# Kernel tuning notes

Measured on AMD Instinct MI355X. Metric: run time of the kernel, lower is better.

## Reference

```python
import jax, jax.numpy as jnp
import numpy as np

N = 12288   # nodes
E = 393216  # edges (avg degree 32)
B = 16      # graphs in batch
F_IN = 15   # node feature dim
H = 32      # hidden_dim
EMB = 64    # embedding_dim
NC = 11     # num_classes
EDIM = 2    # edge feature dim
EPS = 1e-5  # BatchNorm eps


def _bn(x, gamma, beta):
    # training-mode BatchNorm1d: biased batch variance, matches torch normalization
    mu = jnp.mean(x, axis=0)
    var = jnp.var(x, axis=0)
    return gamma * (x - mu) * jax.lax.rsqrt(var + EPS) + beta


def setup_inputs() -> dict:
    key = jax.random.key(0)
    ks = jax.random.split(key, 16)
    def p(k, shape, s=0.05):
        return jax.random.normal(k, shape, dtype=jnp.float32) * s
    z = lambda *s: jnp.zeros(s, jnp.float32)
    o = lambda *s: jnp.ones(s, jnp.float32)
    return {
        "x": jax.random.normal(ks[0], (N, F_IN), dtype=jnp.float32),
        "edge_attr": jax.random.normal(ks[1], (E, EDIM), dtype=jnp.float32),
        "w_edge": p(ks[2], (EDIM, 1)), "b_edge": z(1),
        "w1": p(ks[3], (F_IN, H)), "b1": z(H), "g1": o(H), "be1": z(H),
        "w2": p(ks[4], (H, 2 * H)), "b2": z(2 * H), "g2": o(2 * H), "be2": z(2 * H),
        "w3": p(ks[5], (2 * H, EMB)), "b3": z(EMB), "g3": o(EMB), "be3": z(EMB),
        "wf1": p(ks[6], (EMB, 512)), "bf1": z(512), "gf1": o(512), "bef1": z(512),
        "wf2": p(ks[7], (512, 256)), "bf2": z(256), "gf2": o(256), "bef2": z(256),
        "wf3": p(ks[8], (256, NC)), "bf3": z(NC),
        "edge_index": jax.random.randint(ks[9], (2, E), 0, N, dtype=jnp.int64)
                      if jax.config.jax_enable_x64 else jax.random.randint(ks[9], (2, E), 0, N),
        "batch": jnp.sort(jax.random.randint(ks[10], (N,), 0, B)),
    }


def reference(x, edge_attr, w_edge, b_edge,
              w1, b1, g1, be1, w2, b2, g2, be2, w3, b3, g3, be3,
              wf1, bf1, gf1, bef1, wf2, bf2, gf2, bef2, wf3, bf3,
              edge_index, batch):
    # edge weights: sigmoid(Linear(edge_attr)) -> [E]
    ew = jax.nn.sigmoid(edge_attr @ w_edge + b_edge)[:, 0]
    # dense adjacency with self loops, accumulate duplicates (sparse_coo.to_dense)
    loop = jnp.arange(N)
    row = jnp.concatenate([edge_index[0], loop])
    col = jnp.concatenate([edge_index[1], loop])
    w_aug = jnp.concatenate([ew, jnp.ones((N,), ew.dtype)])
    adj = jnp.zeros((N, N), ew.dtype).at[row, col].add(w_aug)
    # symmetric degree normalization D^-1/2 A D^-1/2
    deg = adj.sum(axis=1)
    dis = jnp.where(deg > 0, jax.lax.rsqrt(jnp.where(deg > 0, deg, 1.0)), 0.0)
    support = dis[:, None] * adj * dis[None, :]
    # three GCN layers: support @ x @ W + b, BN, relu
    h = jax.nn.relu(_bn(support @ x @ w1 + b1, g1, be1))
    h = jax.nn.relu(_bn(support @ h @ w2 + b2, g2, be2))
    h = jax.nn.relu(_bn(support @ h @ w3 + b3, g3, be3))
    # global max pool per graph (empty graphs -> zeros)
    seg = jax.ops.segment_max(h, batch, num_segments=B)
    cnt = jax.ops.segment_sum(jnp.ones((N,), h.dtype), batch, num_segments=B)
    emb = jnp.where(cnt[:, None] > 0, seg, 0.0)
    # MLP head (dropout = identity at inference)
    o = jax.nn.relu(_bn(emb @ wf1 + bf1, gf1, bef1))
    o = jax.nn.relu(_bn(o @ wf2 + bf2, gf2, bef2))
    logits = o @ wf3 + bf3
    return jax.nn.log_softmax(logits, axis=1), emb
```

## Files before the change

kernel.cpp:

```cpp
#include <hip/hip_runtime.h>
#include <hip/hip_bf16.h>

#define NN   12288
#define EE   393216
#define WELL 96
#define NELL (NN*WELL)
#define BG   16
#define FIN  15
#define FH1  32
#define FH2  64
#define NCL  11
#define BNEPS 1e-5f
#define NBANK 32

typedef unsigned long long u64;
static inline int cdiv(long a, long b){ return (int)((a + b - 1) / b); }

__device__ __forceinline__ int getIdx(const void* p, long i, int is64){
  return is64 ? (int)((const long long*)p)[i] : ((const int*)p)[i];
}

__device__ __forceinline__ float degOf(u64 dc){
  return 1.0f + (float)(unsigned)(dc & 0xffffffffull) * (1.0f/1048576.0f);
}

__global__ void k_pre(u64* deg_cnt, uint4* csr_q, float* csp1, float* csp2,
                      float* csp3, const void* ei, const void* batch, int* flags){
  int g = blockIdx.x*256 + threadIdx.x;
  if (g < NELL/2) csr_q[g] = make_uint4(0,0,0,0);
  if (g < NN) deg_cnt[g] = 0ull;
  if (g < NBANK*128){ csp1[g] = 0.f; csp2[g] = 0.f; csp3[g] = 0.f; }
  if (blockIdx.x == 0 && threadIdx.x < 64){
    const int* a = (const int*)ei;
    unsigned long long m0 = __ballot(a[2*threadIdx.x + 1] == 0);
    const int* b = (const int*)batch;
    int j = 96*threadIdx.x;
    unsigned long long m1 = __ballot(b[2*j + 1] == 0);
    if (threadIdx.x == 0){
      flags[0] = (m0 == ~0ull) ? 1 : 0;
      flags[1] = (m1 == ~0ull) ? 1 : 0;
    }
  }
}

__global__ void k_edge(const float* ea, const float* we, const float* bedg,
                       const void* ei, const int* flags, u64* deg_cnt, u64* csr_p){
  int e = blockIdx.x*256 + threadIdx.x;
  if (e >= EE) return;
  int is64 = flags[0];
  float z = ea[2*e]*we[0] + ea[2*e+1]*we[1] + bedg[0];
  float w = 1.0f/(1.0f + expf(-z));
  int r = getIdx(ei, e, is64);
  int c = getIdx(ei, (long)EE + e, is64);
  u64 add = (1ull << 32) | (u64)__float2uint_rn(w * 1048576.0f);
  u64 old = atomicAdd(&deg_cnt[r], add);
  int slot = (int)(old >> 32);
  if (slot < WELL)
    csr_p[r*WELL + slot] = (u64)(unsigned)c | ((u64)__float_as_uint(w) << 32);
}

__global__ void k_fix(u64* csr_p, const u64* deg_cnt){
  int g = blockIdx.x*256 + threadIdx.x;
  if (g >= NELL) return;
  u64 v = csr_p[g];
  unsigned wu = (unsigned)(v >> 32);
  if (wu == 0u) return;
  int c = (int)(unsigned)(v & 0xffffffffull);
  float w = __uint_as_float(wu) * rsqrtf(degOf(deg_cnt[c]));
  ((unsigned*)csr_p)[2*g + 1] = __float_as_uint(w);
}

template<int F, int FP, int FO, int APPLY_BN>
__global__ void __launch_bounds__(256) k_layer(
    const float* __restrict__ Hin, const float* __restrict__ csin,
    const float* __restrict__ g, const float* __restrict__ be,
    const float* __restrict__ W, const float* __restrict__ bias,
    const u64* __restrict__ deg_cnt, const u64* __restrict__ csr_p,
    float* __restrict__ Pout, float* __restrict__ csout){
  const int R = 256/FP;
  __shared__ float At[R][FP];
  __shared__ float lcs[FO], lcq[FO];
  if (threadIdx.x < FO){ lcs[threadIdx.x] = 0.f; lcq[threadIdx.x] = 0.f; }
  int f = threadIdx.x % FP, lr = threadIdx.x / FP;
  float sc = 1.f, sh = 0.f;
  if (APPLY_BN && f < F){
    float s = 0.f, q = 0.f;
    #pragma unroll
    for (int b = 0; b < NBANK; b++){ s += csin[b*128 + f]; q += csin[b*128 + 64 + f]; }
    float mu  = s*(1.0f/NN);
    float var = q*(1.0f/NN) - mu*mu;
    float rinv = rsqrtf(var + BNEPS);
    sc = g[f]*rinv; sh = be[f] - mu*sc;
  }
  int row = blockIdx.x*R + lr;
  if (f < F){
    u64 dc = deg_cnt[row];
    float d = rsqrtf(degOf(dc));
    int n = (int)(dc >> 32);
    float v0 = Hin[row*F + f];
    if (APPLY_BN) v0 = fmaxf(v0*sc + sh, 0.f);
    float acc = d * v0;
    int nch = (n + 7) >> 3;
    const uint4* pb = (const uint4*)(csr_p + row*WELL);
    if (nch > 0){
      uint4 a0 = pb[0], a1 = pb[1], a2 = pb[2], a3 = pb[3];
      for (int ch = 0; ch < nch; ch++){
        uint4 b0, b1, b2, b3;
        bool more = (ch + 1 < nch);
        if (more){ b0 = pb[4*ch+4]; b1 = pb[4*ch+5]; b2 = pb[4*ch+6]; b3 = pb[4*ch+7]; }
        float h0 = Hin[(int)a0.x*F + f];
        float h1 = Hin[(int)a0.z*F + f];
        float h2 = Hin[(int)a1.x*F + f];
        float h3 = Hin[(int)a1.z*F + f];
        float h4 = Hin[(int)a2.x*F + f];
        float h5 = Hin[(int)a2.z*F + f];
        float h6 = Hin[(int)a3.x*F + f];
        float h7 = Hin[(int)a3.z*F + f];
        if (APPLY_BN){
          h0 = fmaxf(h0*sc + sh, 0.f); h1 = fmaxf(h1*sc + sh, 0.f);
          h2 = fmaxf(h2*sc + sh, 0.f); h3 = fmaxf(h3*sc + sh, 0.f);
          h4 = fmaxf(h4*sc + sh, 0.f); h5 = fmaxf(h5*sc + sh, 0.f);
          h6 = fmaxf(h6*sc + sh, 0.f); h7 = fmaxf(h7*sc + sh, 0.f);
        }
        acc += __uint_as_float(a0.y)*h0 + __uint_as_float(a0.w)*h1
             + __uint_as_float(a1.y)*h2 + __uint_as_float(a1.w)*h3
             + __uint_as_float(a2.y)*h4 + __uint_as_float(a2.w)*h5
             + __uint_as_float(a3.y)*h6 + __uint_as_float(a3.w)*h7;
        if (more){ a0 = b0; a1 = b1; a2 = b2; a3 = b3; }
      }
    }
    At[lr][f] = d * acc;
  }
  __syncthreads();
  const int fo = threadIdx.x % FO;
  float bb = bias[fo];
  for (int o = threadIdx.x; o < R*FO; o += 256){
    int l = o / FO;
    float s = bb;
    #pragma unroll
    for (int fi = 0; fi < F; fi++) s += At[l][fi] * W[fi*FO + fo];
    Pout[(blockIdx.x*R + l)*FO + fo] = s;
    atomicAdd(&lcs[fo], s);
    atomicAdd(&lcq[fo], s*s);
  }
  __syncthreads();
  if (threadIdx.x < FO){
    int bank = blockIdx.x & (NBANK-1);
    atomicAdd(&csout[bank*128 + threadIdx.x],      lcs[threadIdx.x]);
    atomicAdd(&csout[bank*128 + 64 + threadIdx.x], lcq[threadIdx.x]);
  }
}

__global__ void k_pool(const float* P3, const float* cs3, const float* g3,
                       const float* be3, const void* batch, const int* flags,
                       float* embf, float* out){
  int is64 = flags[1];
  int b = blockIdx.x;
  int lo = 0, hi = NN;
  while (lo < hi){ int m = (lo+hi)>>1; if (getIdx(batch, m, is64) < b) lo = m+1; else hi = m; }
  int start = lo;
  lo = start; hi = NN;
  while (lo < hi){ int m = (lo+hi)>>1; if (getIdx(batch, m, is64) < b+1) lo = m+1; else hi = m; }
  int end = lo;
  int f = threadIdx.x & 63, grp = threadIdx.x >> 6;
  float s = 0.f, q = 0.f;
  #pragma unroll
  for (int bk = 0; bk < NBANK; bk++){ s += cs3[bk*128 + f]; q += cs3[bk*128 + 64 + f]; }
  float mu  = s*(1.0f/NN);
  float var = q*(1.0f/NN) - mu*mu;
  float rinv = rsqrtf(var + BNEPS);
  float sc = g3[f]*rinv, sh = be3[f] - mu*sc;
  float m = 0.0f;
  for (int i = start + grp; i < end; i += 4)
    m = fmaxf(m, P3[(long)i*FH2 + f]*sc + sh);
  __shared__ float shm[4][64];
  shm[grp][f] = m;
  __syncthreads();
  if (grp == 0){
    float v = fmaxf(fmaxf(shm[0][f], shm[1][f]), fmaxf(shm[2][f], shm[3][f]));
    embf[b*64 + f] = v;
    out[BG*NCL + b*64 + f] = v;
  }
}

__global__ void __launch_bounds__(256) k_fcA(const float* embf, const float* wf1,
    const float* bf1, const float* gf1, const float* bef1, float* s1g){
  int c = blockIdx.x*4 + (threadIdx.x >> 6);
  int l = threadIdx.x & 63;
  float wcol = wf1[l*512 + c];
  float z[BG];
  #pragma unroll
  for (int r = 0; r < BG; r++){
    float v = embf[r*64 + l] * wcol;
    #pragma unroll
    for (int off = 32; off > 0; off >>= 1) v += __shfl_down(v, off);
    z[r] = v;
  }
  if (l == 0){
    float bb = bf1[c];
    float s = 0.f, q = 0.f;
    #pragma unroll
    for (int r = 0; r < BG; r++){ float zr = z[r] + bb; s += zr; q += zr*zr; }
    float mean = s*(1.f/BG), var = q*(1.f/BG) - mean*mean;
    float inv = rsqrtf(var + BNEPS);
    float gg = gf1[c], b2 = bef1[c];
    #pragma unroll
    for (int r = 0; r < BG; r++)
      s1g[r*512 + c] = fmaxf(gg*(z[r] + bb - mean)*inv + b2, 0.f);
  }
}

__global__ void __launch_bounds__(256) k_fcB(const float* s1g, const float* wf2,
    const float* bf2, const float* gf2, const float* bef2, float* s2g){
  int c = blockIdx.x*4 + (threadIdx.x >> 6);
  int l = threadIdx.x & 63;
  float wreg[8];
  #pragma unroll
  for (int j = 0; j < 8; j++) wreg[j] = wf2[(l + 64*j)*256 + c];
  float z[BG];
  #pragma unroll
  for (int r = 0; r < BG; r++){
    float v = 0.f;
    #pragma unroll
    for (int j = 0; j < 8; j++) v += s1g[r*512 + l + 64*j] * wreg[j];
    #pragma unroll
    for (int off = 32; off > 0; off >>= 1) v += __shfl_down(v, off);
    z[r] = v;
  }
  if (l == 0){
    float bb = bf2[c];
    float s = 0.f, q = 0.f;
    #pragma unroll
    for (int r = 0; r < BG; r++){ float zr = z[r] + bb; s += zr; q += zr*zr; }
    float mean = s*(1.f/BG), var = q*(1.f/BG) - mean*mean;
    float inv = rsqrtf(var + BNEPS);
    float gg = gf2[c], b2 = bef2[c];
    #pragma unroll
    for (int r = 0; r < BG; r++)
      s2g[r*256 + c] = fmaxf(gg*(z[r] + bb - mean)*inv + b2, 0.f);
  }
}

__global__ void k_fc3(const float* s2g, const float* wf3, const float* bf3, float* out){
  __shared__ float s2[BG*256];
  __shared__ float sl[BG*NCL];
  int t = threadIdx.x;
  for (int i = t; i < BG*256; i += 256) s2[i] = s2g[i];
  __syncthreads();
  if (t < BG*NCL){
    int r = t / NCL, c = t - r*NCL;
    float s = bf3[c];
    for (int k = 0; k < 256; k++) s += s2[r*256 + k]*wf3[k*NCL + c];
    sl[t] = s;
  }
  __syncthreads();
  if (t < BG){
    float m = -1e30f;
    for (int c = 0; c < NCL; c++) m = fmaxf(m, sl[t*NCL + c]);
    float s = 0.f;
    for (int c = 0; c < NCL; c++) s += expf(sl[t*NCL + c] - m);
    float lg = logf(s) + m;
    for (int c = 0; c < NCL; c++) out[t*NCL + c] = sl[t*NCL + c] - lg;
  }
}

extern "C" void kernel_launch(void* const* d_in, const int* in_sizes, int n_in,
                              void* d_out, int out_size, void* d_ws, size_t ws_size,
                              hipStream_t stream){
  const float* x    = (const float*)d_in[0];
  const float* ea   = (const float*)d_in[1];
  const float* we   = (const float*)d_in[2];
  const float* bedg = (const float*)d_in[3];
  const float* w1   = (const float*)d_in[4];  const float* b1  = (const float*)d_in[5];
  const float* g1   = (const float*)d_in[6];  const float* be1 = (const float*)d_in[7];
  const float* w2   = (const float*)d_in[8];  const float* b2  = (const float*)d_in[9];
  const float* g2   = (const float*)d_in[10]; const float* be2 = (const float*)d_in[11];
  const float* w3   = (const float*)d_in[12]; const float* b3  = (const float*)d_in[13];
  const float* g3   = (const float*)d_in[14]; const float* be3 = (const float*)d_in[15];
  const float* wf1  = (const float*)d_in[16]; const float* bf1 = (const float*)d_in[17];
  const float* gf1  = (const float*)d_in[18]; const float* bef1= (const float*)d_in[19];
  const float* wf2  = (const float*)d_in[20]; const float* bf2 = (const float*)d_in[21];
  const float* gf2  = (const float*)d_in[22]; const float* bef2= (const float*)d_in[23];
  const float* wf3  = (const float*)d_in[24]; const float* bf3 = (const float*)d_in[25];
  const void* ei    = d_in[26];
  const void* batch = d_in[27];
  float* out = (float*)d_out;

  u64* wq = (u64*)d_ws;
  u64* deg_cnt = wq; wq += NN;
  u64* csr_p   = wq; wq += NELL;
  float* ws = (float*)wq;
  float* P1    = ws; ws += NN*FH1;
  float* P2    = ws; ws += NN*FH2;
  float* P3    = ws; ws += NN*FH2;
  float* csp1  = ws; ws += NBANK*128;
  float* csp2  = ws; ws += NBANK*128;
  float* csp3  = ws; ws += NBANK*128;
  float* embf  = ws; ws += BG*64;
  float* s1g   = ws; ws += BG*512;
  float* s2g   = ws; ws += BG*256;
  int* flags   = (int*)ws;

  k_pre<<<cdiv(NELL/2,256), 256, 0, stream>>>(deg_cnt, (uint4*)csr_p,
                                              csp1, csp2, csp3, ei, batch, flags);
  k_edge<<<cdiv(EE,256), 256, 0, stream>>>(ea, we, bedg, ei, flags, deg_cnt, csr_p);
  k_fix<<<cdiv(NELL,256), 256, 0, stream>>>(csr_p, deg_cnt);

  k_layer<FIN,16,FH1,0><<<NN/16, 256, 0, stream>>>(x, nullptr, nullptr, nullptr,
      w1, b1, deg_cnt, csr_p, P1, csp1);
  k_layer<FH1,32,FH2,1><<<NN/8, 256, 0, stream>>>(P1, csp1, g1, be1,
      w2, b2, deg_cnt, csr_p, P2, csp2);
  k_layer<FH2,64,FH2,1><<<NN/4, 256, 0, stream>>>(P2, csp2, g2, be2,
      w3, b3, deg_cnt, csr_p, P3, csp3);

  k_pool<<<BG, 256, 0, stream>>>(P3, csp3, g3, be3, batch, flags, embf, out);
  k_fcA<<<128, 256, 0, stream>>>(embf, wf1, bf1, gf1, bef1, s1g);
  k_fcB<<<64, 256, 0, stream>>>(s1g, wf2, bf2, gf2, bef2, s2g);
  k_fc3<<<1, 256, 0, stream>>>(s2g, wf3, bf3, out);
}
```

Measured before the change: 265.7 us.

## Drop ELL zero-fill, bound slots by degree count, fuse MLP tail cooperatively

The full zeroing pass over the padded ELL adjacency buffer is removed. k_fix and the layer gathers now bound each row by its atomic edge count and mask stale slots, instead of relying on zero-filled entries. The ELL width grows to 128 so row offsets can be computed with shifts. The pool and three MLP kernels are merged into one 16-block cooperative kernel that uses grid syncs, cutting launch overhead, and the edge-attribute read is vectorized. The cost is a larger workspace and extra per-chunk masking branches in the layer kernels.

```diff
diff --git a/kernel.cpp b/kernel.cpp
--- a/kernel.cpp
+++ b/kernel.cpp
@@ -1,9 +1,12 @@
 #include <hip/hip_runtime.h>
+#include <hip/hip_cooperative_groups.h>
 #include <hip/hip_bf16.h>
+
+namespace cg = cooperative_groups;
 
 #define NN   12288
 #define EE   393216
-#define WELL 96
+#define WELL 128
 #define NELL (NN*WELL)
 #define BG   16
 #define FIN  15
@@ -24,10 +27,9 @@
   return 1.0f + (float)(unsigned)(dc & 0xffffffffull) * (1.0f/1048576.0f);
 }
 
-__global__ void k_pre(u64* deg_cnt, uint4* csr_q, float* csp1, float* csp2,
-                      float* csp3, const void* ei, const void* batch, int* flags){
+__global__ void k_pre(u64* deg_cnt, float* csp1, float* csp2, float* csp3,
+                      const void* ei, const void* batch, int* flags){
   int g = blockIdx.x*256 + threadIdx.x;
-  if (g < NELL/2) csr_q[g] = make_uint4(0,0,0,0);
   if (g < NN) deg_cnt[g] = 0ull;
   if (g < NBANK*128){ csp1[g] = 0.f; csp2[g] = 0.f; csp3[g] = 0.f; }
   if (blockIdx.x == 0 && threadIdx.x < 64){
@@ -48,7 +50,8 @@
   int e = blockIdx.x*256 + threadIdx.x;
   if (e >= EE) return;
   int is64 = flags[0];
-  float z = ea[2*e]*we[0] + ea[2*e+1]*we[1] + bedg[0];
+  float2 eav = ((const float2*)ea)[e];
+  float z = eav.x*we[0] + eav.y*we[1] + bedg[0];
   float w = 1.0f/(1.0f + expf(-z));
   int r = getIdx(ei, e, is64);
   int c = getIdx(ei, (long)EE + e, is64);
@@ -56,17 +59,19 @@
   u64 old = atomicAdd(&deg_cnt[r], add);
   int slot = (int)(old >> 32);
   if (slot < WELL)
-    csr_p[r*WELL + slot] = (u64)(unsigned)c | ((u64)__float_as_uint(w) << 32);
+    csr_p[(r << 7) + slot] = (u64)(unsigned)c | ((u64)__float_as_uint(w) << 32);
 }
 
 __global__ void k_fix(u64* csr_p, const u64* deg_cnt){
   int g = blockIdx.x*256 + threadIdx.x;
   if (g >= NELL) return;
+  int row = g >> 7, s = g & (WELL-1);
+  int n = (int)(deg_cnt[row] >> 32);
+  n = n < WELL ? n : WELL;
+  if (s >= n) return;
   u64 v = csr_p[g];
-  unsigned wu = (unsigned)(v >> 32);
-  if (wu == 0u) return;
   int c = (int)(unsigned)(v & 0xffffffffull);
-  float w = __uint_as_float(wu) * rsqrtf(degOf(deg_cnt[c]));
+  float w = __uint_as_float((unsigned)(v >> 32)) * rsqrtf(degOf(deg_cnt[c]));
   ((unsigned*)csr_p)[2*g + 1] = __float_as_uint(w);
 }
 
@@ -97,17 +102,29 @@
     u64 dc = deg_cnt[row];
     float d = rsqrtf(degOf(dc));
     int n = (int)(dc >> 32);
+    n = n < WELL ? n : WELL;
     float v0 = Hin[row*F + f];
     if (APPLY_BN) v0 = fmaxf(v0*sc + sh, 0.f);
     float acc = d * v0;
     int nch = (n + 7) >> 3;
-    const uint4* pb = (const uint4*)(csr_p + row*WELL);
+    const uint4* pb = (const uint4*)(csr_p + ((long)row << 7));
     if (nch > 0){
       uint4 a0 = pb[0], a1 = pb[1], a2 = pb[2], a3 = pb[3];
       for (int ch = 0; ch < nch; ch++){
         uint4 b0, b1, b2, b3;
         bool more = (ch + 1 < nch);
         if (more){ b0 = pb[4*ch+4]; b1 = pb[4*ch+5]; b2 = pb[4*ch+6]; b3 = pb[4*ch+7]; }
+        int base = ch*8;
+        if (base + 8 > n){
+          if (base+0 >= n){ a0.x = 0u; a0.y = 0u; }
+          if (base+1 >= n){ a0.z = 0u; a0.w = 0u; }
+          if (base+2 >= n){ a1.x = 0u; a1.y = 0u; }
+          if (base+3 >= n){ a1.z = 0u; a1.w = 0u; }
+          if (base+4 >= n){ a2.x = 0u; a2.y = 0u; }
+          if (base+5 >= n){ a2.z = 0u; a2.w = 0u; }
+          if (base+6 >= n){ a3.x = 0u; a3.y = 0u; }
+          if (base+7 >= n){ a3.z = 0u; a3.w = 0u; }
+        }
         float h0 = Hin[(int)a0.x*F + f];
         float h1 = Hin[(int)a0.z*F + f];
         float h2 = Hin[(int)a1.x*F + f];
@@ -151,116 +168,138 @@
   }
 }
 
-__global__ void k_pool(const float* P3, const float* cs3, const float* g3,
-                       const float* be3, const void* batch, const int* flags,
-                       float* embf, float* out){
-  int is64 = flags[1];
-  int b = blockIdx.x;
-  int lo = 0, hi = NN;
-  while (lo < hi){ int m = (lo+hi)>>1; if (getIdx(batch, m, is64) < b) lo = m+1; else hi = m; }
-  int start = lo;
-  lo = start; hi = NN;
-  while (lo < hi){ int m = (lo+hi)>>1; if (getIdx(batch, m, is64) < b+1) lo = m+1; else hi = m; }
-  int end = lo;
-  int f = threadIdx.x & 63, grp = threadIdx.x >> 6;
-  float s = 0.f, q = 0.f;
-  #pragma unroll
-  for (int bk = 0; bk < NBANK; bk++){ s += cs3[bk*128 + f]; q += cs3[bk*128 + 64 + f]; }
-  float mu  = s*(1.0f/NN);
-  float var = q*(1.0f/NN) - mu*mu;
-  float rinv = rsqrtf(var + BNEPS);
-  float sc = g3[f]*rinv, sh = be3[f] - mu*sc;
-  float m = 0.0f;
-  for (int i = start + grp; i < end; i += 4)
-    m = fmaxf(m, P3[(long)i*FH2 + f]*sc + sh);
-  __shared__ float shm[4][64];
-  shm[grp][f] = m;
-  __syncthreads();
-  if (grp == 0){
-    float v = fmaxf(fmaxf(shm[0][f], shm[1][f]), fmaxf(shm[2][f], shm[3][f]));
-    embf[b*64 + f] = v;
-    out[BG*NCL + b*64 + f] = v;
-  }
-}
-
-__global__ void __launch_bounds__(256) k_fcA(const float* embf, const float* wf1,
-    const float* bf1, const float* gf1, const float* bef1, float* s1g){
-  int c = blockIdx.x*4 + (threadIdx.x >> 6);
-  int l = threadIdx.x & 63;
-  float wcol = wf1[l*512 + c];
-  float z[BG];
-  #pragma unroll
-  for (int r = 0; r < BG; r++){
-    float v = embf[r*64 + l] * wcol;
-    #pragma unroll
-    for (int off = 32; off > 0; off >>= 1) v += __shfl_down(v, off);
-    z[r] = v;
-  }
-  if (l == 0){
-    float bb = bf1[c];
+struct TailP {
+  const float *P3, *cs3, *g3, *be3;
+  const void *batch; const int *flags;
+  const float *wf1,*bf1,*gf1,*bef1,*wf2,*bf2,*gf2,*bef2,*wf3,*bf3;
+  float *embf, *s1g, *s2g, *out;
+};
+
+__global__ void __launch_bounds__(256) k_tail(TailP p){
+  cg::grid_group grid = cg::this_grid();
+  const int b = blockIdx.x, t = threadIdx.x;
+  __shared__ float shpool[4][64];
+  __shared__ float semb[BG*64];
+  __shared__ float s1l[BG*512];
+  __shared__ float s2l[256];
+  __shared__ float sl[NCL];
+
+  {
+    int is64 = p.flags[1];
+    int lo = 0, hi = NN;
+    while (lo < hi){ int m = (lo+hi)>>1; if (getIdx(p.batch, m, is64) < b) lo = m+1; else hi = m; }
+    int start = lo;
+    lo = start; hi = NN;
+    while (lo < hi){ int m = (lo+hi)>>1; if (getIdx(p.batch, m, is64) < b+1) lo = m+1; else hi = m; }
+    int end = lo;
+    int f = t & 63, grp = t >> 6;
     float s = 0.f, q = 0.f;
     #pragma unroll
-    for (int r = 0; r < BG; r++){ float zr = z[r] + bb; s += zr; q += zr*zr; }
-    float mean = s*(1.f/BG), var = q*(1.f/BG) - mean*mean;
-    float inv = rsqrtf(var + BNEPS);
-    float gg = gf1[c], b2 = bef1[c];
-    #pragma unroll
-    for (int r = 0; r < BG; r++)
-      s1g[r*512 + c] = fmaxf(gg*(z[r] + bb - mean)*inv + b2, 0.f);
-  }
-}
-
-__global__ void __launch_bounds__(256) k_fcB(const float* s1g, const float* wf2,
-    const float* bf2, const float* gf2, const float* bef2, float* s2g){
-  int c = blockIdx.x*4 + (threadIdx.x >> 6);
-  int l = threadIdx.x & 63;
-  float wreg[8];
-  #pragma unroll
-  for (int j = 0; j < 8; j++) wreg[j] = wf2[(l + 64*j)*256 + c];
-  float z[BG];
-  #pragma unroll
-  for (int r = 0; r < BG; r++){
-    float v = 0.f;
-    #pragma unroll
-    for (int j = 0; j < 8; j++) v += s1g[r*512 + l + 64*j] * wreg[j];
-    #pragma unroll
-    for (int off = 32; off > 0; off >>= 1) v += __shfl_down(v, off);
-    z[r] = v;
-  }
-  if (l == 0){
-    float bb = bf2[c];
-    float s = 0.f, q = 0.f;
-    #pragma unroll
-    for (int r = 0; r < BG; r++){ float zr = z[r] + bb; s += zr; q += zr*zr; }
-    float mean = s*(1.f/BG), var = q*(1.f/BG) - mean*mean;
-    float inv = rsqrtf(var + BNEPS);
-    float gg = gf2[c], b2 = bef2[c];
-    #pragma unroll
-    for (int r = 0; r < BG; r++)
-      s2g[r*256 + c] = fmaxf(gg*(z[r] + bb - mean)*inv + b2, 0.f);
-  }
-}
-
-__global__ void k_fc3(const float* s2g, const float* wf3, const float* bf3, float* out){
-  __shared__ float s2[BG*256];
-  __shared__ float sl[BG*NCL];
-  int t = threadIdx.x;
-  for (int i = t; i < BG*256; i += 256) s2[i] = s2g[i];
-  __syncthreads();
-  if (t < BG*NCL){
-    int r = t / NCL, c = t - r*NCL;
-    float s = bf3[c];
-    for (int k = 0; k < 256; k++) s += s2[r*256 + k]*wf3[k*NCL + c];
-    sl[t] = s;
-  }
-  __syncthreads();
-  if (t < BG){
+    for (int bk = 0; bk < NBANK; bk++){ s += p.cs3[bk*128 + f]; q += p.cs3[bk*128 + 64 + f]; }
+    float mu  = s*(1.0f/NN);
+    float var = q*(1.0f/NN) - mu*mu;
+    float rinv = rsqrtf(var + BNEPS);
+    float sc = p.g3[f]*rinv, sh = p.be3[f] - mu*sc;
+    float m = 0.0f;
+    for (int i = start + grp; i < end; i += 4)
+      m = fmaxf(m, p.P3[(long)i*FH2 + f]*sc + sh);
+    shpool[grp][f] = m;
+    __syncthreads();
+    if (grp == 0){
+      float v = fmaxf(fmaxf(shpool[0][f], shpool[1][f]), fmaxf(shpool[2][f], shpool[3][f]));
+      p.embf[b*64 + f] = v;
+      p.out[BG*NCL + b*64 + f] = v;
+    }
+  }
+  grid.sync();
+
+  for (int i = t; i < BG*64; i += 256) semb[i] = p.embf[i];
+  __syncthreads();
+  {
+    int wv = t >> 6, l = t & 63;
+    for (int i = 0; i < 8; i++){
+      int c = b*32 + wv*8 + i;
+      float wcol = p.wf1[l*512 + c];
+      float z[BG];
+      #pragma unroll
+      for (int r = 0; r < BG; r++){
+        float v = semb[r*64 + l] * wcol;
+        #pragma unroll
+        for (int off = 32; off > 0; off >>= 1) v += __shfl_down(v, off);
+        z[r] = v;
+      }
+      if (l == 0){
+        float bb = p.bf1[c];
+        float s = 0.f, q = 0.f;
+        #pragma unroll
+        for (int r = 0; r < BG; r++){ float zr = z[r] + bb; s += zr; q += zr*zr; }
+        float mean = s*(1.f/BG), var = q*(1.f/BG) - mean*mean;
+        float inv = rsqrtf(var + BNEPS);
+        float gg = p.gf1[c], b2 = p.bef1[c];
+        #pragma unroll
+        for (int r = 0; r < BG; r++)
+          p.s1g[r*512 + c] = fmaxf(gg*(z[r] + bb - mean)*inv + b2, 0.f);
+      }
+    }
+  }
+  grid.sync();
+
+  for (int i = t; i < BG*512; i += 256) s1l[i] = p.s1g[i];
+  __syncthreads();
+  {
+    int wv = t >> 6, l = t & 63;
+    for (int i = 0; i < 4; i++){
+      int c = b*16 + wv*4 + i;
+      float wr[8];
+      #pragma unroll
+      for (int j = 0; j < 8; j++) wr[j] = p.wf2[(l + 64*j)*256 + c];
+      float z[BG];
+      #pragma unroll
+      for (int r = 0; r < BG; r++){
+        float v = 0.f;
+        #pragma unroll
+        for (int j = 0; j < 8; j++) v += s1l[r*512 + l + 64*j] * wr[j];
+        #pragma unroll
+        for (int off = 32; off > 0; off >>= 1) v += __shfl_down(v, off);
+        z[r] = v;
+      }
+      if (l == 0){
+        float bb = p.bf2[c];
+        float s = 0.f, q = 0.f;
+        #pragma unroll
+        for (int r = 0; r < BG; r++){ float zr = z[r] + bb; s += zr; q += zr*zr; }
+        float mean = s*(1.f/BG), var = q*(1.f/BG) - mean*mean;
+        float inv = rsqrtf(var + BNEPS);
+        float gg = p.gf2[c], b2 = p.bef2[c];
+        #pragma unroll
+        for (int r = 0; r < BG; r++)
+          p.s2g[r*256 + c] = fmaxf(gg*(z[r] + bb - mean)*inv + b2, 0.f);
+      }
+    }
+  }
+  grid.sync();
+
+  for (int i = t; i < 256; i += 256) s2l[i] = p.s2g[b*256 + i];
+  __syncthreads();
+  {
+    int wv = t >> 6, l = t & 63;
+    for (int cc = wv; cc < NCL; cc += 4){
+      float v = 0.f;
+      #pragma unroll
+      for (int j = 0; j < 4; j++) v += s2l[l + 64*j] * p.wf3[(l + 64*j)*NCL + cc];
+      #pragma unroll
+      for (int off = 32; off > 0; off >>= 1) v += __shfl_down(v, off);
+      if (l == 0) sl[cc] = v + p.bf3[cc];
+    }
+  }
+  __syncthreads();
+  if (t == 0){
     float m = -1e30f;
-    for (int c = 0; c < NCL; c++) m = fmaxf(m, sl[t*NCL + c]);
+    for (int c = 0; c < NCL; c++) m = fmaxf(m, sl[c]);
     float s = 0.f;
-    for (int c = 0; c < NCL; c++) s += expf(sl[t*NCL + c] - m);
+    for (int c = 0; c < NCL; c++) s += expf(sl[c] - m);
     float lg = logf(s) + m;
-    for (int c = 0; c < NCL; c++) out[t*NCL + c] = sl[t*NCL + c] - lg;
+    for (int c = 0; c < NCL; c++) p.out[b*NCL + c] = sl[c] - lg;
   }
 }
 
@@ -301,8 +340,7 @@
   float* s2g   = ws; ws += BG*256;
   int* flags   = (int*)ws;
 
-  k_pre<<<cdiv(NELL/2,256), 256, 0, stream>>>(deg_cnt, (uint4*)csr_p,
-                                              csp1, csp2, csp3, ei, batch, flags);
+  k_pre<<<48, 256, 0, stream>>>(deg_cnt, csp1, csp2, csp3, ei, batch, flags);
   k_edge<<<cdiv(EE,256), 256, 0, stream>>>(ea, we, bedg, ei, flags, deg_cnt, csr_p);
   k_fix<<<cdiv(NELL,256), 256, 0, stream>>>(csr_p, deg_cnt);
 
@@ -313,8 +351,13 @@
   k_layer<FH2,64,FH2,1><<<NN/4, 256, 0, stream>>>(P2, csp2, g2, be2,
       w3, b3, deg_cnt, csr_p, P3, csp3);
 
-  k_pool<<<BG, 256, 0, stream>>>(P3, csp3, g3, be3, batch, flags, embf, out);
-  k_fcA<<<128, 256, 0, stream>>>(embf, wf1, bf1, gf1, bef1, s1g);
-  k_fcB<<<64, 256, 0, stream>>>(s1g, wf2, bf2, gf2, bef2, s2g);
-  k_fc3<<<1, 256, 0, stream>>>(s2g, wf3, bf3, out);
-}
+  TailP tp;
+  tp.P3 = P3; tp.cs3 = csp3; tp.g3 = g3; tp.be3 = be3;
+  tp.batch = batch; tp.flags = flags;
+  tp.wf1 = wf1; tp.bf1 = bf1; tp.gf1 = gf1; tp.bef1 = bef1;
+  tp.wf2 = wf2; tp.bf2 = bf2; tp.gf2 = gf2; tp.bef2 = bef2;
+  tp.wf3 = wf3; tp.bf3 = bf3;
+  tp.embf = embf; tp.s1g = s1g; tp.s2g = s2g; tp.out = out;
+  void* targs[] = { &tp };
+  hipLaunchCooperativeKernel((const void*)k_tail, dim3(BG), dim3(256), targs, 0, stream);
+}
```

Result: slower. 325.9 us (+22.6%).
